# Optimization experiments

Measured on AMD Instinct MI355X. Metric: run time of the kernel, lower is better.

## Reference

```python
import jax, jax.numpy as jnp
import numpy as np

B, D, H = 4096, 256, 1024
TRACE_STEPS = 10
T_FINAL = 1.0


def setup_inputs() -> dict:
    key = jax.random.key(0)
    k0, k1, k2 = jax.random.split(key, 3)
    s1 = 1.0 / np.sqrt(D + 1)
    s2 = 1.0 / np.sqrt(H)
    return {
        "x": jax.random.normal(k0, (B, D), dtype=jnp.float32),
        "W1": jax.random.uniform(k1, (D + 1, H), jnp.float32, -s1, s1),
        "b1": jnp.zeros((H,), jnp.float32),
        "W2": jax.random.uniform(k2, (H, D), jnp.float32, -s2, s2),
        "b2": jnp.zeros((D,), jnp.float32),
    }


def _odefun(params, t, z):
    # FFJORD vector field: tanh MLP on [z, t]. z: [B, D] -> [B, D]
    W1, b1, W2, b2 = params
    tcol = jnp.full((z.shape[0], 1), t, dtype=z.dtype)
    h = jnp.tanh(jnp.concatenate([z, tcol], axis=-1) @ W1 + b1)
    return h @ W2 + b2


def _rademacher(key, shape, dtype):
    # randint(0,2)*2-1, matching the torch probe construction
    return jax.random.randint(key, shape, 0, 2).astype(dtype) * 2.0 - 1.0


def _aug_dynamics(params, t, state, e):
    # state: [B, D+1] = [z | logp]; e: [TRACE_STEPS, B, D] Rademacher probes.
    # torch computes etf = grad((f*e).sum(), z) = e^T J, div = (e^T J)*e summed.
    # e^T J e == e . (J e), so forward-mode jvp gives identical math.
    z = state[:, :-1]
    f = lambda zz: _odefun(params, t, zz)

    def probe(ei):
        f_z, Je = jax.jvp(f, (z,), (ei,))
        return f_z, jnp.sum(Je * ei, axis=-1)  # [B]

    f_z, divs = jax.vmap(probe)(e)
    f_z = f_z[0]                       # primal identical across probes
    div_est = jnp.mean(divs, axis=0)   # average of trace_steps estimates
    return jnp.concatenate([f_z, -div_est[:, None]], axis=-1)


def reference(x, W1, b1, W2, b2):
    params = (W1, b1, W2, b2)
    Bx = x.shape[0]
    ekey = jax.random.key(42)
    probes = lambda i: _rademacher(jax.random.fold_in(ekey, i), (TRACE_STEPS, Bx, D), x.dtype)

    # initial augmented state: [z, logp=0]
    y0 = jnp.concatenate([x, jnp.zeros((Bx, 1), x.dtype)], axis=-1)

    # t_grid = [0, T] with 2 points -> fixed-grid rk4 takes ONE RK4 step of size T
    h = T_FINAL
    g = lambda t, y, i: _aug_dynamics(params, t, y, probes(i))
    k1 = g(0.0, y0, 0)
    k2 = g(0.5 * h, y0 + 0.5 * h * k1, 1)
    k3 = g(0.5 * h, y0 + 0.5 * h * k2, 2)
    k4 = g(h, y0 + h * k3, 3)
    y1 = y0 + (h / 6.0) * (k1 + 2.0 * k2 + 2.0 * k3 + k4)

    # module returns the full trajectory `output`: [len(t_grid), B, D+1]
    return jnp.stack([y0, y1], axis=0)
```

## Files before the change

kernel.cpp:

```cpp
#include <hip/hip_runtime.h>
#include <stdint.h>

#define BATCH 4096
#define DIMD  256
#define DIMH  1024
#define NEEL  10485760
#define NSLOT 1310720

typedef __attribute__((ext_vector_type(8))) short short8;
typedef __attribute__((ext_vector_type(4))) float float4v;

struct Keys4 { uint32_t a[4]; uint32_t b[4]; };

__host__ __device__ static inline uint32_t rotl32(uint32_t v, int r) {
#ifdef __HIP_DEVICE_COMPILE__
    return __builtin_amdgcn_alignbit(v, v, 32 - r);
#else
    return (v << r) | (v >> (32 - r));
#endif
}

__host__ __device__ static inline void tf2x32(uint32_t k0, uint32_t k1,
                                              uint32_t c0, uint32_t c1,
                                              uint32_t& o0, uint32_t& o1) {
    uint32_t ks0 = k0, ks1 = k1, ks2 = k0 ^ k1 ^ 0x1BD11BDAu;
    uint32_t x0 = c0 + ks0, x1 = c1 + ks1;
#define TF_R4(a, b, c, d)                                   \
    x0 += x1; x1 = rotl32(x1, a); x1 ^= x0;                 \
    x0 += x1; x1 = rotl32(x1, b); x1 ^= x0;                 \
    x0 += x1; x1 = rotl32(x1, c); x1 ^= x0;                 \
    x0 += x1; x1 = rotl32(x1, d); x1 ^= x0;
    TF_R4(13, 15, 26, 6)  x0 += ks1; x1 += ks2 + 1u;
    TF_R4(17, 29, 16, 24) x0 += ks2; x1 += ks0 + 2u;
    TF_R4(13, 15, 26, 6)  x0 += ks0; x1 += ks1 + 3u;
    TF_R4(17, 29, 16, 24) x0 += ks1; x1 += ks2 + 4u;
    TF_R4(13, 15, 26, 6)  x0 += ks2; x1 += ks0 + 5u;
#undef TF_R4
    o0 = x0; o1 = x1;
}

__device__ static inline short f2bf(float f) {
    uint32_t u = __float_as_uint(f);
    uint32_t r = (u + 0x7FFFu + ((u >> 16) & 1u)) >> 16;
    return (short)r;
}

__device__ static inline void async_cp16(const void* gsrc, void* ldst) {
    typedef __attribute__((address_space(1))) const unsigned int GU;
    typedef __attribute__((address_space(3))) unsigned int LU;
    __builtin_amdgcn_global_load_lds((GU*)gsrc, (LU*)ldst, 16, 0, 0);
}

__device__ static inline void egen_slot(short* __restrict__ EF, uint32_t q,
                                        uint32_t k0, uint32_t k1) {
    const uint32_t lane = q & 63u;
    const uint32_t ks   = (q >> 6) & 7u;
    const uint32_t T    = (q >> 9) & 255u;
    const uint32_t probe = q >> 17;
    const uint32_t b = T * 16u + (lane & 15u);
    const uint32_t d0 = ks * 32u + (lane >> 4) * 8u;
    const uint32_t jbase = (probe * 4096u + b) * 256u + d0;
    short8 val;
#pragma unroll
    for (int jj = 0; jj < 8; ++jj) {
        uint32_t y0, y1;
        tf2x32(k0, k1, 0u, jbase + (uint32_t)jj, y0, y1);
        val[jj] = ((y0 ^ y1) & 1u) ? (short)0x3F80 : (short)0xBF80u;
    }
    *(short8*)&EF[(size_t)q * 8] = val;
}

__global__ __launch_bounds__(256) void k_prep(
    const float* __restrict__ x,  const float* __restrict__ W1,
    const float* __restrict__ W2, short* __restrict__ W1T,
    short* __restrict__ W2B, short* __restrict__ W2T,
    short* __restrict__ zb, float* __restrict__ dv,
    short* __restrict__ E0, uint32_t ek0, uint32_t ek1)
{
    const int idx = blockIdx.x * 256 + threadIdx.x;
    if (idx < 262144) {
        const int n = idx >> 8, d = idx & 255;
        W1T[idx] = f2bf(W1[d * DIMH + n]);
    } else if (idx < 524288) {
        const int i = idx - 262144;
        W2B[i] = f2bf(W2[i]);
    } else if (idx < 786432) {
        const int i = idx - 524288;
        const int d = i >> 10, k = i & 1023;
        W2T[i] = f2bf(W2[k * DIMD + d]);
    } else if (idx < 1835008) {
        const int i = idx - 786432;
        zb[i] = f2bf(x[i]);
    } else if (idx < 1851392) {
        dv[idx - 1835008] = 0.0f;
    } else {
        egen_slot(E0, (uint32_t)(idx - 1851392), ek0, ek1);
    }
}

__global__ __launch_bounds__(256) void k_pre_div(
    const short* __restrict__ Zb, const short* __restrict__ W1T,
    const short* __restrict__ W2B, const float* __restrict__ W1,
    const float* __restrict__ b1, float tval,
    const short* __restrict__ Ecur, short* __restrict__ h_bf,
    float* __restrict__ divacc,
    short* __restrict__ Enext, uint32_t nk0, uint32_t nk1, int do_egen)
{
    __shared__ short8 Es[2][2048];
    const int t = threadIdx.x;
    const int b0 = blockIdx.x * 64;
    const int nt = blockIdx.y;
    const int wave = t >> 6, lane = t & 63;
    const int col = lane & 15, kq = lane >> 4;
    const int n = nt * 64 + wave * 16 + col;
    const int Tb = b0 >> 4;

    const short8* Ebase = (const short8*)Ecur;
    auto stage = [&](int p) {
        const short8* src = Ebase + (size_t)(p * 256 + Tb) * 512 + wave * 64;
        short8* dst = &Es[p & 1][wave * 64];
#pragma unroll
        for (int k = 0; k < 8; ++k)
            async_cp16(src + k * 256 + lane, dst + k * 256);
    };
    stage(0);
    stage(1);

    const uint32_t bflat = (uint32_t)(blockIdx.y * 64 + blockIdx.x);
    const uint32_t qbase = bflat * 256u + (uint32_t)t;
    if (do_egen) egen_slot(Enext, qbase, nk0, nk1);

    short8 bufr[8], bvfr[8];
#pragma unroll
    for (int ks = 0; ks < 8; ++ks) {
        bufr[ks] = *(const short8*)&W1T[n * DIMD + ks * 32 + kq * 8];
        bvfr[ks] = *(const short8*)&W2B[n * DIMD + ks * 32 + kq * 8];
    }

    float sreg[4][4];
    const float add = tval * W1[DIMD * DIMH + n] + b1[n];
#pragma unroll
    for (int ms = 0; ms < 4; ++ms) {
        float4v acc = {0.f, 0.f, 0.f, 0.f};
#pragma unroll
        for (int ks = 0; ks < 8; ++ks) {
            short8 af = *(const short8*)&Zb[(b0 + ms * 16 + col) * DIMD + ks * 32 + kq * 8];
            acc = __builtin_amdgcn_mfma_f32_16x16x32_bf16(af, bufr[ks], acc, 0, 0, 0);
        }
#pragma unroll
        for (int r = 0; r < 4; ++r) {
            float hv = tanhf(acc[r] + add);
            h_bf[(b0 + ms * 16 + kq * 4 + r) * DIMH + n] = f2bf(hv);
            sreg[ms][r] = 1.0f - hv * hv;
        }
    }

    float rowacc[4][4];
#pragma unroll
    for (int a = 0; a < 4; ++a)
#pragma unroll
        for (int r = 0; r < 4; ++r) rowacc[a][r] = 0.0f;

#pragma unroll 1
    for (int pp = 0; pp < 10; ++pp) {
        if (pp < 9) { asm volatile("s_waitcnt vmcnt(8)" ::: "memory"); }
        else        { asm volatile("s_waitcnt vmcnt(0)" ::: "memory"); }
        __builtin_amdgcn_s_barrier();

        const short8* buf = (const short8*)Es[pp & 1];
#pragma unroll
        for (int ms = 0; ms < 4; ++ms) {
            float4v u = {0.f, 0.f, 0.f, 0.f}, v = {0.f, 0.f, 0.f, 0.f};
#pragma unroll
            for (int ks = 0; ks < 8; ++ks) {
                short8 af = buf[ms * 512 + ks * 64 + lane];
                u = __builtin_amdgcn_mfma_f32_16x16x32_bf16(af, bufr[ks], u, 0, 0, 0);
                v = __builtin_amdgcn_mfma_f32_16x16x32_bf16(af, bvfr[ks], v, 0, 0, 0);
            }
#pragma unroll
            for (int r = 0; r < 4; ++r)
                rowacc[ms][r] += u[r] * sreg[ms][r] * v[r];
        }

        asm volatile("" ::: "memory");
        __builtin_amdgcn_s_barrier();
        if (pp < 8) stage(pp + 2);
        if (do_egen && (pp & 1) == 0 && pp <= 6)
            egen_slot(Enext, qbase + (uint32_t)(1 + (pp >> 1)) * 262144u, nk0, nk1);
    }

#pragma unroll
    for (int ms = 0; ms < 4; ++ms) {
#pragma unroll
        for (int r = 0; r < 4; ++r) {
            float p = rowacc[ms][r];
            p += __shfl_xor(p, 1, 64);
            p += __shfl_xor(p, 2, 64);
            p += __shfl_xor(p, 4, 64);
            p += __shfl_xor(p, 8, 64);
            rowacc[ms][r] = p;
        }
    }
    if (col == 0) {
#pragma unroll
        for (int ms = 0; ms < 4; ++ms)
#pragma unroll
            for (int r = 0; r < 4; ++r)
                atomicAdd(&divacc[b0 + ms * 16 + kq * 4 + r], rowacc[ms][r] * 0.1f);
    }
}

__global__ __launch_bounds__(256) void k_fz2(
    const short* __restrict__ Hb, const short* __restrict__ W2T,
    const float* __restrict__ b2, const float* __restrict__ x,
    float* __restrict__ rksum, float cw, int first,
    float cnext, int write_zb, short* __restrict__ zb,
    int final_out, const float* __restrict__ dv, float* __restrict__ out)
{
    const int t = threadIdx.x;
    const int wave = t >> 6, lane = t & 63;
    const int col = lane & 15, kq = lane >> 4;
    const int m0 = blockIdx.x * 16;
    const int n0 = blockIdx.y * 64 + wave * 16;
    const int TOT = BATCH * (DIMD + 1);
    const float sixth = 1.0f / 6.0f;

    float4v acc = {0.f, 0.f, 0.f, 0.f};

    const short* ap = &Hb[(m0 + col) * DIMH + kq * 8];
    const short* bp = &W2T[(n0 + col) * DIMH + kq * 8];
    short8 a_cur = *(const short8*)ap;
    short8 b_cur = *(const short8*)bp;

    for (int ks = 0; ks < 31; ++ks) {
        short8 a_nxt = *(const short8*)&ap[(ks + 1) * 32];
        short8 b_nxt = *(const short8*)&bp[(ks + 1) * 32];
        acc = __builtin_amdgcn_mfma_f32_16x16x32_bf16(a_cur, b_cur, acc, 0, 0, 0);
        a_cur = a_nxt;
        b_cur = b_nxt;
    }
    acc = __builtin_amdgcn_mfma_f32_16x16x32_bf16(a_cur, b_cur, acc, 0, 0, 0);

    {
        const int nn = n0 + col;
        const float bias = b2[nn];
#pragma unroll
        for (int r = 0; r < 4; ++r) {
            const int m = m0 + kq * 4 + r;
            const int o = m * DIMD + nn;
            const float val = acc[r] + bias;
            if (final_out) {
                const float xv = x[o];
                out[m * (DIMD + 1) + nn] = xv;
                out[TOT + m * (DIMD + 1) + nn] =
                    xv + (rksum[o] + val) * sixth;
            } else {
                const float contrib = cw * val;
                rksum[o] = first ? contrib : (rksum[o] + contrib);
                if (write_zb)
                    zb[o] = f2bf(x[o] + cnext * val);
            }
        }
    }

    if (final_out && blockIdx.y == 0 && wave == 0 && col == 0) {
#pragma unroll
        for (int r = 0; r < 4; ++r) {
            const int m = m0 + kq * 4 + r;
            const float d1 = dv[m];
            const float d2 = dv[BATCH + m];
            const float d3 = dv[2 * BATCH + m];
            const float d4 = dv[3 * BATCH + m];
            out[m * (DIMD + 1) + DIMD] = 0.0f;
            out[TOT + m * (DIMD + 1) + DIMD] =
                -(d1 + 2.0f * d2 + 2.0f * d3 + d4) * sixth;
        }
    }
}

extern "C" void kernel_launch(void* const* d_in, const int* in_sizes, int n_in,
                              void* d_out, int out_size, void* d_ws, size_t ws_size,
                              hipStream_t stream) {
    const float* x  = (const float*)d_in[0];
    const float* W1 = (const float*)d_in[1];
    const float* b1 = (const float*)d_in[2];
    const float* W2 = (const float*)d_in[3];
    const float* b2 = (const float*)d_in[4];
    float* out = (float*)d_out;

    char* ws = (char*)d_ws;
    short* hb    = (short*)(ws);
    float* rksum = (float*)(ws + 8388608);
    short* zb    = (short*)(ws + 12582912);
    short* w1t   = (short*)(ws + 14680064);
    short* w2b   = (short*)(ws + 15204352);
    short* w2t   = (short*)(ws + 15728640);
    float* dv    = (float*)(ws + 16252928);
    short* e0    = (short*)(ws + 16318464);
    short* e1    = (short*)(ws + 37289984);

    Keys4 keys;
    for (uint32_t i = 0; i < 4; ++i) {
        uint32_t f0, f1, g0, g1;
        tf2x32(0u, 42u, 0u, i, f0, f1);
        tf2x32(f0, f1, 0u, 1u, g0, g1);
        keys.a[i] = g0;
        keys.b[i] = g1;
    }

    k_prep<<<12352, 256, 0, stream>>>(x, W1, W2, w1t, w2b, w2t, zb, dv,
                                      e0, keys.a[0], keys.b[0]);

    const float tvals[4] = {0.0f, 0.5f, 0.5f, 1.0f};
    const float cnext[4] = {0.5f, 0.5f, 1.0f, 0.0f};
    const float cw[4]    = {1.0f, 2.0f, 2.0f, 1.0f};
    for (int s = 0; s < 4; ++s) {
        const int last = (s == 3);
        short* ecur = (s & 1) ? e1 : e0;
        short* enxt = (s & 1) ? e0 : e1;
        k_pre_div<<<dim3(64, 16), 256, 0, stream>>>(
            zb, w1t, w2b, W1, b1, tvals[s], ecur,
            hb, dv + (size_t)s * BATCH,
            enxt, last ? 0u : keys.a[s + 1], last ? 0u : keys.b[s + 1],
            last ? 0 : 1);
        k_fz2<<<dim3(256, 4), 256, 0, stream>>>(hb, w2t, b2, x, rksum,
                                                cw[s], (s == 0) ? 1 : 0,
                                                cnext[s], (s < 3) ? 1 : 0, zb,
                                                last ? 1 : 0, dv, out);
    }
}
```

Measured before the change: 490.2 us.

## Replace LDS-staged probe loads with register double-buffered global prefetch and swizzled grid

The div kernel no longer stages Rademacher probe tiles into shared memory with async copies and barriers. Each wave now loads its own probe fragments straight from global memory into two alternating register buffers, prefetching the next sub-tile while running MFMAs on the current one. The launch grid becomes 1D with a swizzled block-to-tile mapping so neighbouring blocks share batch tiles for L2 reuse, and probe generation for the next stage is redistributed across the loop. This removes LDS traffic and barriers but raises register pressure and relies on per-wave global loads hiding latency.

```diff
diff --git a/kernel.cpp b/kernel.cpp
--- a/kernel.cpp
+++ b/kernel.cpp
@@ -43,12 +43,6 @@
     uint32_t u = __float_as_uint(f);
     uint32_t r = (u + 0x7FFFu + ((u >> 16) & 1u)) >> 16;
     return (short)r;
-}
-
-__device__ static inline void async_cp16(const void* gsrc, void* ldst) {
-    typedef __attribute__((address_space(1))) const unsigned int GU;
-    typedef __attribute__((address_space(3))) unsigned int LU;
-    __builtin_amdgcn_global_load_lds((GU*)gsrc, (LU*)ldst, 16, 0, 0);
 }
 
 __device__ static inline void egen_slot(short* __restrict__ EF, uint32_t q,
@@ -106,29 +100,26 @@
     float* __restrict__ divacc,
     short* __restrict__ Enext, uint32_t nk0, uint32_t nk1, int do_egen)
 {
-    __shared__ short8 Es[2][2048];
     const int t = threadIdx.x;
-    const int b0 = blockIdx.x * 64;
-    const int nt = blockIdx.y;
+    const uint32_t L = blockIdx.x;
+    const int s_bt = (int)((L & 7u) | ((L >> 7) << 3));
+    const int nt   = (int)((L >> 3) & 15u);
+    const int b0 = s_bt * 64;
     const int wave = t >> 6, lane = t & 63;
     const int col = lane & 15, kq = lane >> 4;
     const int n = nt * 64 + wave * 16 + col;
-    const int Tb = b0 >> 4;
-
-    const short8* Ebase = (const short8*)Ecur;
-    auto stage = [&](int p) {
-        const short8* src = Ebase + (size_t)(p * 256 + Tb) * 512 + wave * 64;
-        short8* dst = &Es[p & 1][wave * 64];
-#pragma unroll
-        for (int k = 0; k < 8; ++k)
-            async_cp16(src + k * 256 + lane, dst + k * 256);
-    };
-    stage(0);
-    stage(1);
-
-    const uint32_t bflat = (uint32_t)(blockIdx.y * 64 + blockIdx.x);
-    const uint32_t qbase = bflat * 256u + (uint32_t)t;
-    if (do_egen) egen_slot(Enext, qbase, nk0, nk1);
+    const int Tb = s_bt * 4;
+
+    const short8* Ew = (const short8*)Ecur + (size_t)Tb * 512 + lane;
+
+#define LOADG(DST, PP, MS) do {                                         \
+        const short8* _src = Ew + ((size_t)(PP) * 256 + (MS)) * 512;    \
+        _Pragma("unroll")                                               \
+        for (int _k = 0; _k < 8; ++_k) DST[_k] = _src[_k * 64];         \
+    } while (0)
+
+    short8 ea[8], eb[8];
+    LOADG(ea, 0, 0);
 
     short8 bufr[8], bvfr[8];
 #pragma unroll
@@ -161,33 +152,34 @@
 #pragma unroll
         for (int r = 0; r < 4; ++r) rowacc[a][r] = 0.0f;
 
+    const uint32_t bflat = (uint32_t)(nt * 64 + s_bt);
+    const uint32_t qbase = bflat * 256u + (uint32_t)t;
+
+#define MSTEP(CUR, NXT, NPP, NMS, MS, DOPF) do {                        \
+        if (DOPF) LOADG(NXT, NPP, NMS);                                 \
+        float4v u = {0.f, 0.f, 0.f, 0.f}, v = {0.f, 0.f, 0.f, 0.f};     \
+        _Pragma("unroll")                                               \
+        for (int _ks = 0; _ks < 8; ++_ks) {                             \
+            u = __builtin_amdgcn_mfma_f32_16x16x32_bf16(CUR[_ks], bufr[_ks], u, 0, 0, 0); \
+            v = __builtin_amdgcn_mfma_f32_16x16x32_bf16(CUR[_ks], bvfr[_ks], v, 0, 0, 0); \
+        }                                                               \
+        _Pragma("unroll")                                               \
+        for (int _r = 0; _r < 4; ++_r)                                  \
+            rowacc[MS][_r] += u[_r] * sreg[MS][_r] * v[_r];             \
+    } while (0)
+
 #pragma unroll 1
     for (int pp = 0; pp < 10; ++pp) {
-        if (pp < 9) { asm volatile("s_waitcnt vmcnt(8)" ::: "memory"); }
-        else        { asm volatile("s_waitcnt vmcnt(0)" ::: "memory"); }
-        __builtin_amdgcn_s_barrier();
-
-        const short8* buf = (const short8*)Es[pp & 1];
-#pragma unroll
-        for (int ms = 0; ms < 4; ++ms) {
-            float4v u = {0.f, 0.f, 0.f, 0.f}, v = {0.f, 0.f, 0.f, 0.f};
-#pragma unroll
-            for (int ks = 0; ks < 8; ++ks) {
-                short8 af = buf[ms * 512 + ks * 64 + lane];
-                u = __builtin_amdgcn_mfma_f32_16x16x32_bf16(af, bufr[ks], u, 0, 0, 0);
-                v = __builtin_amdgcn_mfma_f32_16x16x32_bf16(af, bvfr[ks], v, 0, 0, 0);
-            }
-#pragma unroll
-            for (int r = 0; r < 4; ++r)
-                rowacc[ms][r] += u[r] * sreg[ms][r] * v[r];
-        }
-
-        asm volatile("" ::: "memory");
-        __builtin_amdgcn_s_barrier();
-        if (pp < 8) stage(pp + 2);
-        if (do_egen && (pp & 1) == 0 && pp <= 6)
-            egen_slot(Enext, qbase + (uint32_t)(1 + (pp >> 1)) * 262144u, nk0, nk1);
-    }
+        if (do_egen && !(pp & 1))
+            egen_slot(Enext, qbase + (uint32_t)(pp >> 1) * 262144u, nk0, nk1);
+        MSTEP(ea, eb, pp, 1, 0, 1);
+        MSTEP(eb, ea, pp, 2, 1, 1);
+        MSTEP(ea, eb, pp, 3, 2, 1);
+        if (pp < 9) { MSTEP(eb, ea, pp + 1, 0, 3, 1); }
+        else        { MSTEP(eb, ea, 0, 0, 3, 0); }
+    }
+#undef MSTEP
+#undef LOADG
 
 #pragma unroll
     for (int ms = 0; ms < 4; ++ms) {
@@ -318,7 +310,7 @@
         const int last = (s == 3);
         short* ecur = (s & 1) ? e1 : e0;
         short* enxt = (s & 1) ? e0 : e1;
-        k_pre_div<<<dim3(64, 16), 256, 0, stream>>>(
+        k_pre_div<<<1024, 256, 0, stream>>>(
             zb, w1t, w2b, W1, b1, tvals[s], ecur,
             hb, dv + (size_t)s * BATCH,
             enxt, last ? 0u : keys.a[s + 1], last ? 0u : keys.b[s + 1],
```

Result: slower. 638.3 us (+30.2%).

## Widen pre_div blocks to 512 threads and stage two probes per synchronous LDS load

Applied to the files above, without the earlier changes.

The divergence kernel now uses 512-thread blocks covering 128 hidden columns, which halves the grid and lets each probe tile staged in shared memory feed twice as many waves. The async global_load_lds double buffer is replaced by plain synchronous copies of two probes per iteration, bracketed by __syncthreads. Probe generation for the next stage moves to the top of each of the five iterations. The aim is more reuse of each staged probe tile and fewer barriers, at the cost of losing overlap between loads and MFMA work.

```diff
diff --git a/kernel.cpp b/kernel.cpp
--- a/kernel.cpp
+++ b/kernel.cpp
@@ -43,12 +43,6 @@
     uint32_t u = __float_as_uint(f);
     uint32_t r = (u + 0x7FFFu + ((u >> 16) & 1u)) >> 16;
     return (short)r;
-}
-
-__device__ static inline void async_cp16(const void* gsrc, void* ldst) {
-    typedef __attribute__((address_space(1))) const unsigned int GU;
-    typedef __attribute__((address_space(3))) unsigned int LU;
-    __builtin_amdgcn_global_load_lds((GU*)gsrc, (LU*)ldst, 16, 0, 0);
 }
 
 __device__ static inline void egen_slot(short* __restrict__ EF, uint32_t q,
@@ -98,7 +92,7 @@
     }
 }
 
-__global__ __launch_bounds__(256) void k_pre_div(
+__global__ __launch_bounds__(512, 4) void k_pre_div(
     const short* __restrict__ Zb, const short* __restrict__ W1T,
     const short* __restrict__ W2B, const float* __restrict__ W1,
     const float* __restrict__ b1, float tval,
@@ -106,29 +100,13 @@
     float* __restrict__ divacc,
     short* __restrict__ Enext, uint32_t nk0, uint32_t nk1, int do_egen)
 {
-    __shared__ short8 Es[2][2048];
+    __shared__ short8 Es[4096];
     const int t = threadIdx.x;
     const int b0 = blockIdx.x * 64;
-    const int nt = blockIdx.y;
+    const int ntp = blockIdx.y;
     const int wave = t >> 6, lane = t & 63;
     const int col = lane & 15, kq = lane >> 4;
-    const int n = nt * 64 + wave * 16 + col;
-    const int Tb = b0 >> 4;
-
-    const short8* Ebase = (const short8*)Ecur;
-    auto stage = [&](int p) {
-        const short8* src = Ebase + (size_t)(p * 256 + Tb) * 512 + wave * 64;
-        short8* dst = &Es[p & 1][wave * 64];
-#pragma unroll
-        for (int k = 0; k < 8; ++k)
-            async_cp16(src + k * 256 + lane, dst + k * 256);
-    };
-    stage(0);
-    stage(1);
-
-    const uint32_t bflat = (uint32_t)(blockIdx.y * 64 + blockIdx.x);
-    const uint32_t qbase = bflat * 256u + (uint32_t)t;
-    if (do_egen) egen_slot(Enext, qbase, nk0, nk1);
+    const int n = ntp * 128 + wave * 16 + col;
 
     short8 bufr[8], bvfr[8];
 #pragma unroll
@@ -161,32 +139,43 @@
 #pragma unroll
         for (int r = 0; r < 4; ++r) rowacc[a][r] = 0.0f;
 
+    const uint32_t bflat = (uint32_t)(blockIdx.y * 64 + blockIdx.x);
+    const uint32_t qbase = bflat * 512u + (uint32_t)t;
+
+    const int Tb = b0 >> 4;
+
 #pragma unroll 1
-    for (int pp = 0; pp < 10; ++pp) {
-        if (pp < 9) { asm volatile("s_waitcnt vmcnt(8)" ::: "memory"); }
-        else        { asm volatile("s_waitcnt vmcnt(0)" ::: "memory"); }
-        __builtin_amdgcn_s_barrier();
-
-        const short8* buf = (const short8*)Es[pp & 1];
-#pragma unroll
-        for (int ms = 0; ms < 4; ++ms) {
-            float4v u = {0.f, 0.f, 0.f, 0.f}, v = {0.f, 0.f, 0.f, 0.f};
-#pragma unroll
-            for (int ks = 0; ks < 8; ++ks) {
-                short8 af = buf[ms * 512 + ks * 64 + lane];
-                u = __builtin_amdgcn_mfma_f32_16x16x32_bf16(af, bufr[ks], u, 0, 0, 0);
-                v = __builtin_amdgcn_mfma_f32_16x16x32_bf16(af, bvfr[ks], v, 0, 0, 0);
+    for (int pp = 0; pp < 5; ++pp) {
+        if (do_egen) {
+            egen_slot(Enext, qbase + (uint32_t)pp * 262144u, nk0, nk1);
+        }
+        const short8* src0 = (const short8*)Ecur + (size_t)((2 * pp) * 256 + Tb) * 512;
+        const short8* src1 = src0 + (size_t)256 * 512;
+        __syncthreads();
+#pragma unroll
+        for (int k = 0; k < 4; ++k)
+            Es[t + k * 512] = src0[t + k * 512];
+#pragma unroll
+        for (int k = 0; k < 4; ++k)
+            Es[2048 + t + k * 512] = src1[t + k * 512];
+        __syncthreads();
+
+#pragma unroll
+        for (int half = 0; half < 2; ++half) {
+#pragma unroll
+            for (int ms = 0; ms < 4; ++ms) {
+                float4v u = {0.f, 0.f, 0.f, 0.f}, v = {0.f, 0.f, 0.f, 0.f};
+#pragma unroll
+                for (int ks = 0; ks < 8; ++ks) {
+                    short8 af = Es[half * 2048 + ((ms * 8 + ks) << 6) + lane];
+                    u = __builtin_amdgcn_mfma_f32_16x16x32_bf16(af, bufr[ks], u, 0, 0, 0);
+                    v = __builtin_amdgcn_mfma_f32_16x16x32_bf16(af, bvfr[ks], v, 0, 0, 0);
+                }
+#pragma unroll
+                for (int r = 0; r < 4; ++r)
+                    rowacc[ms][r] += u[r] * sreg[ms][r] * v[r];
             }
-#pragma unroll
-            for (int r = 0; r < 4; ++r)
-                rowacc[ms][r] += u[r] * sreg[ms][r] * v[r];
-        }
-
-        asm volatile("" ::: "memory");
-        __builtin_amdgcn_s_barrier();
-        if (pp < 8) stage(pp + 2);
-        if (do_egen && (pp & 1) == 0 && pp <= 6)
-            egen_slot(Enext, qbase + (uint32_t)(1 + (pp >> 1)) * 262144u, nk0, nk1);
+        }
     }
 
 #pragma unroll
@@ -318,7 +307,7 @@
         const int last = (s == 3);
         short* ecur = (s & 1) ? e1 : e0;
         short* enxt = (s & 1) ? e0 : e1;
-        k_pre_div<<<dim3(64, 16), 256, 0, stream>>>(
+        k_pre_div<<<dim3(64, 8), 512, 0, stream>>>(
             zb, w1t, w2b, W1, b1, tvals[s], ecur,
             hb, dv + (size_t)s * BATCH,
             enxt, last ? 0u : keys.a[s + 1], last ? 0u : keys.b[s + 1],
```

Result: slower. 534.8 us (+9.1%).
